# Performance work log

Measured on AMD Instinct MI355X. Metric: run time of the kernel, lower is better.

The kernel has to match this reference:

```python
import jax, jax.numpy as jnp
import numpy as np

N1, N2, P, D = 32, 64, 196, 128


def setup_inputs() -> dict:
    key = jax.random.key(0)
    k1, k2, k3 = jax.random.split(key, 3)
    return {
        "features": jax.random.normal(k1, (N1, P, D), jnp.float32),
        "normal_features": jax.random.normal(k2, (N2, P, D), jnp.float32),
        "background_masks": jax.random.uniform(k3, (N1, P), jnp.float32),
        "PH": 14, "PW": 14, "H": 224, "W": 224,
    }


def _interp1d(x, out_size, axis):
    """1-D bilinear resize along `axis`, matching torch align_corners=False."""
    in_size = x.shape[axis]
    src = jnp.maximum((jnp.arange(out_size) + 0.5) * (in_size / out_size) - 0.5, 0.0)
    i0 = jnp.clip(jnp.floor(src).astype(jnp.int32), 0, in_size - 1)
    i1 = jnp.minimum(i0 + 1, in_size - 1)
    w = (src - i0).astype(x.dtype)
    x0 = jnp.take(x, i0, axis=axis)
    x1 = jnp.take(x, i1, axis=axis)
    shape = [1] * x.ndim
    shape[axis] = out_size
    w = w.reshape(shape)
    return x0 * (1.0 - w) + x1 * w


def reference(features, normal_features, background_masks, PH, PW, H, W):
    # L2-normalize patch features
    f = features / jnp.linalg.norm(features, axis=-1, keepdims=True)      # [N1,P,D]
    nf = normal_features / jnp.linalg.norm(normal_features, axis=-1, keepdims=True)  # [N2,P,D]
    # cdist on unit vectors: ||a-b|| = sqrt(2 - 2 a.b); then /2 as in source
    sim = jnp.einsum('apd,bqd->abpq', f, nf)                              # [N1,N2,P,P]
    dist = jnp.sqrt(jnp.maximum(2.0 - 2.0 * sim, 0.0)) * 0.5
    scores_patch = dist.min(axis=-1)                                      # [N1,N2,P]
    scores_patch = scores_patch * background_masks[:, None, :]
    scores = scores_patch.max(axis=-1)                                    # [N1,N2]
    scores_patch = scores_patch.mean(axis=1)                              # [N1,P]
    n1 = features.shape[0]
    sp = scores_patch.reshape(n1, PH, PW)
    sp = _interp1d(sp, H, axis=1)
    scores_pixel = _interp1d(sp, W, axis=2)                               # [N1,H,W]
    return scores.mean(axis=-1), scores_pixel
```

## Files before the change

kernel.cpp:

```cpp
#include <hip/hip_runtime.h>
#include <hip/hip_fp16.h>

typedef __attribute__((ext_vector_type(8))) short f16x8;
typedef __attribute__((ext_vector_type(8))) _Float16 half8;
typedef __attribute__((ext_vector_type(4))) float f32x4;

__device__ __forceinline__ unsigned short f2h(float x) {
    __half h = __float2half(x);
    unsigned short u;
    __builtin_memcpy(&u, &h, 2);
    return u;
}

__device__ __forceinline__ void gll16(const void* g, void* l) {
    __builtin_amdgcn_global_load_lds(
        (const __attribute__((address_space(1))) unsigned*)g,
        (__attribute__((address_space(3))) unsigned*)l, 16, 0, 0);
}

__global__ __launch_bounds__(256) void norm_kernel(
    const float* __restrict__ feats, const float* __restrict__ nfeats,
    unsigned short* __restrict__ fH, unsigned short* __restrict__ nfH)
{
    int row  = blockIdx.x * 4 + (threadIdx.x >> 6);
    int lane = threadIdx.x & 63;
    const float* src;
    unsigned short* dst;
    if (row < 6272) { src = feats  + (size_t)row * 128; dst = fH  + (size_t)row * 128; }
    else { int r2 = row - 6272; src = nfeats + (size_t)r2 * 128; dst = nfH + (size_t)r2 * 128; }

    float2 v = *(const float2*)(src + lane * 2);
    float ss = v.x * v.x + v.y * v.y;
    #pragma unroll
    for (int m = 1; m < 64; m <<= 1) ss += __shfl_xor(ss, m, 64);
    float rn = rsqrtf(ss);
    ushort2 o; o.x = f2h(v.x * rn); o.y = f2h(v.y * rn);
    *(ushort2*)(dst + lane * 2) = o;
}

__device__ __forceinline__ void stage196(const f16x8* __restrict__ g, f16x8* l,
                                         int tid, int wave) {
    #pragma unroll
    for (int i = 0; i < 6; ++i) {
        int slot = i * 512 + tid;
        int row = slot >> 4, cc = slot & 15;
        gll16(g + row * 16 + (cc ^ (row & 7)), l + i * 512 + wave * 64);
    }
    if (tid < 64) {
        int slot = 3072 + tid;
        int row = slot >> 4, cc = slot & 15;
        gll16(g + row * 16 + (cc ^ (row & 7)), l + 3072);
    }
}

__global__ __launch_bounds__(512, 2) void simmax_kernel(
    const unsigned short* __restrict__ fH, const unsigned short* __restrict__ nfH,
    const float* __restrict__ mask, float* __restrict__ sp, float* __restrict__ scores)
{
    __shared__ f16x8 lds[3 * 3136];
    __shared__ unsigned smaxL[8 * 208];
    __shared__ unsigned scoresL[8];
    f16x8* Fl = lds;
    f16x8* B0 = lds + 3136;
    f16x8* B1 = lds + 6272;

    int a = blockIdx.x & 31, bg = blockIdx.x >> 5;
    int b0 = bg * 8;
    int tid = threadIdx.x, wave = tid >> 6, lane = tid & 63;
    int l15 = lane & 15, lg = lane >> 4;
    int pg = wave & 1, qs = wave >> 1;
    int p0 = pg ? 68 : 0;
    const int qstart[4] = {0, 4, 7, 10};
    const int qend[4]   = {4, 7, 10, 13};

    stage196((const f16x8*)(fH  + (size_t)a  * 196 * 128), Fl, tid, wave);
    stage196((const f16x8*)(nfH + (size_t)b0 * 196 * 128), B0, tid, wave);
    for (int i = tid; i < 8 * 208; i += 512) smaxL[i] = 0u;
    if (tid < 8) scoresL[tid] = 0u;
    __syncthreads();

    half8 pb[8][4];
    #pragma unroll
    for (int pt = 0; pt < 8; ++pt) {
        int row = p0 + pt * 16 + l15;
        #pragma unroll
        for (int ks = 0; ks < 4; ++ks) {
            pb[pt][ks] = *(const half8*)(Fl + ((row << 4) | ((ks * 4 + lg) ^ (row & 7))));
            asm volatile("" : "+v"(pb[pt][ks]));
        }
    }

    for (int bi = 0; bi < 8; ++bi) {
        f16x8* Bcur = (bi & 1) ? B1 : B0;
        f16x8* Bnxt = (bi & 1) ? B0 : B1;
        if (bi < 7)
            stage196((const f16x8*)(nfH + (size_t)(b0 + bi + 1) * 196 * 128), Bnxt, tid, wave);

        float rmax[8];
        #pragma unroll
        for (int pt = 0; pt < 8; ++pt) rmax[pt] = -3.0f;

        for (int qi = qstart[qs]; qi < qend[qs]; ++qi) {
            int qbase = (qi < 12) ? qi * 16 : 180;
            f32x4 acc[8];
            #pragma unroll
            for (int pt = 0; pt < 8; ++pt) acc[pt] = (f32x4){0.f, 0.f, 0.f, 0.f};
            #pragma unroll
            for (int ks = 0; ks < 4; ++ks) {
                int row = qbase + l15;
                half8 qa = *(const half8*)(Bcur + ((row << 4) | ((ks * 4 + lg) ^ (row & 7))));
                #pragma unroll
                for (int pt = 0; pt < 8; ++pt)
                    acc[pt] = __builtin_amdgcn_mfma_f32_16x16x32_f16(qa, pb[pt][ks], acc[pt], 0, 0, 0);
            }
            #pragma unroll
            for (int pt = 0; pt < 8; ++pt)
                rmax[pt] = fmaxf(rmax[pt],
                           fmaxf(fmaxf(acc[pt][0], acc[pt][1]),
                                 fmaxf(acc[pt][2], acc[pt][3])));
        }
        #pragma unroll
        for (int pt = 0; pt < 8; ++pt)
            atomicMax(&smaxL[bi * 208 + p0 + pt * 16 + l15],
                      __float_as_uint(rmax[pt] + 3.0f));

        __syncthreads();
    }

    if (wave < 4) {
        int p = tid;
        float mk = (p < 196) ? mask[a * 196 + p] : 0.0f;
        float d8[8];
        #pragma unroll
        for (int bi = 0; bi < 8; ++bi) {
            float d = 0.0f;
            if (p < 196) {
                float sim = __uint_as_float(smaxL[bi * 208 + p]) - 3.0f;
                d = 0.5f * sqrtf(fmaxf(2.0f - 2.0f * sim, 0.0f)) * mk;
            }
            d8[bi] = d;
            float m = d;
            #pragma unroll
            for (int s = 1; s < 64; s <<= 1) m = fmaxf(m, __shfl_xor(m, s, 64));
            if (lane == 0) atomicMax(&scoresL[bi], __float_as_uint(m));
        }
        if (p < 196) {
            float* dst = sp + ((size_t)a * 196 + p) * 64 + b0;
            *(f32x4*)(dst)     = (f32x4){d8[0], d8[1], d8[2], d8[3]};
            *(f32x4*)(dst + 4) = (f32x4){d8[4], d8[5], d8[6], d8[7]};
        }
    }
    __syncthreads();
    if (tid < 8)
        scores[a * 64 + b0 + tid] = __uint_as_float(scoresL[tid]);
}

__global__ __launch_bounds__(256) void patchmean_kernel(
    const float* __restrict__ sp, const float* __restrict__ scores,
    float* __restrict__ patch, float* __restrict__ out)
{
    int a = blockIdx.x, tid = threadIdx.x;
    if (tid < 196) {
        const f32x4* v = (const f32x4*)(sp + ((size_t)a * 196 + tid) * 64);
        float s = 0.0f;
        #pragma unroll
        for (int j = 0; j < 16; ++j) { f32x4 x = v[j]; s += x[0] + x[1] + x[2] + x[3]; }
        patch[a * 196 + tid] = s * (1.0f / 64.0f);
    }
    if (tid >= 192 && tid < 256) {
        int l = tid - 192;
        float s = scores[a * 64 + l];
        #pragma unroll
        for (int m = 1; m < 64; m <<= 1) s += __shfl_xor(s, m, 64);
        if (l == 0) out[a] = s * (1.0f / 64.0f);
    }
}

__global__ __launch_bounds__(256) void upsample_kernel(
    const float* __restrict__ patch, float* __restrict__ out)
{
    int bid = blockIdx.x;
    int a = bid / 28, band = bid % 28;
    __shared__ float pt[196];
    if (threadIdx.x < 196) pt[threadIdx.x] = patch[a * 196 + threadIdx.x];
    __syncthreads();

    float* op = out + 32 + (size_t)a * 50176 + band * 8 * 224;
    for (int t = threadIdx.x; t < 8 * 224; t += 256) {
        int h = band * 8 + (t / 224), w = t % 224;
        float sh = fmaxf((h + 0.5f) * 0.0625f - 0.5f, 0.0f);
        float sw = fmaxf((w + 0.5f) * 0.0625f - 0.5f, 0.0f);
        int h0 = (int)sh, w0 = (int)sw;
        int h1 = min(h0 + 1, 13), w1 = min(w0 + 1, 13);
        float fh = sh - (float)h0, fw = sw - (float)w0;
        float v00 = pt[h0 * 14 + w0], v01 = pt[h0 * 14 + w1];
        float v10 = pt[h1 * 14 + w0], v11 = pt[h1 * 14 + w1];
        op[t] = (1.0f - fh) * ((1.0f - fw) * v00 + fw * v01)
              +         fh  * ((1.0f - fw) * v10 + fw * v11);
    }
}

extern "C" void kernel_launch(void* const* d_in, const int* in_sizes, int n_in,
                              void* d_out, int out_size, void* d_ws, size_t ws_size,
                              hipStream_t stream) {
    const float* feats  = (const float*)d_in[0];
    const float* nfeats = (const float*)d_in[1];
    const float* mask   = (const float*)d_in[2];
    float* out = (float*)d_out;

    char* w = (char*)d_ws;
    unsigned short* fH  = (unsigned short*)(w);
    unsigned short* nfH = (unsigned short*)(w + 1605632);
    float* sp     = (float*)(w + 4816896);
    float* scores = (float*)(w + 6422528);
    float* patch  = (float*)(w + 6430720);

    norm_kernel<<<4704, 256, 0, stream>>>(feats, nfeats, fH, nfH);
    simmax_kernel<<<256, 512, 0, stream>>>(fH, nfH, mask, sp, scores);
    patchmean_kernel<<<32, 256, 0, stream>>>(sp, scores, patch, out);
    upsample_kernel<<<896, 256, 0, stream>>>(patch, out);
}
```

Baseline: 49.04 us.

## Drop LDS staging in simmax; load MFMA operands directly from global memory

The similarity-max kernel no longer stages features through LDS with async global-to-LDS copies and double buffering. Each lane now reads its MFMA fragments directly from global memory, relying on the L2/L1 caches for the heavy reuse of the normal-feature rows. The work split is also changed: 512 blocks each handle 4 normal images, waves are arranged as 4 patch groups by 2 query halves, and the launch bound now targets higher occupancy. In exchange, global and cache traffic rises and the B operand loads are uncoalesced per-lane 16-byte reads, which may expose memory latency.

Result: slower. 75.87 us (+54.7%).

```diff
diff --git a/kernel.cpp b/kernel.cpp
--- a/kernel.cpp
+++ b/kernel.cpp
@@ -1,7 +1,6 @@
 #include <hip/hip_runtime.h>
 #include <hip/hip_fp16.h>
 
-typedef __attribute__((ext_vector_type(8))) short f16x8;
 typedef __attribute__((ext_vector_type(8))) _Float16 half8;
 typedef __attribute__((ext_vector_type(4))) float f32x4;
 
@@ -10,12 +9,6 @@
     unsigned short u;
     __builtin_memcpy(&u, &h, 2);
     return u;
-}
-
-__device__ __forceinline__ void gll16(const void* g, void* l) {
-    __builtin_amdgcn_global_load_lds(
-        (const __attribute__((address_space(1))) unsigned*)g,
-        (__attribute__((address_space(3))) unsigned*)l, 16, 0, 0);
 }
 
 __global__ __launch_bounds__(256) void norm_kernel(
@@ -38,120 +31,89 @@
     *(ushort2*)(dst + lane * 2) = o;
 }
 
-__device__ __forceinline__ void stage196(const f16x8* __restrict__ g, f16x8* l,
-                                         int tid, int wave) {
-    #pragma unroll
-    for (int i = 0; i < 6; ++i) {
-        int slot = i * 512 + tid;
-        int row = slot >> 4, cc = slot & 15;
-        gll16(g + row * 16 + (cc ^ (row & 7)), l + i * 512 + wave * 64);
-    }
-    if (tid < 64) {
-        int slot = 3072 + tid;
-        int row = slot >> 4, cc = slot & 15;
-        gll16(g + row * 16 + (cc ^ (row & 7)), l + 3072);
-    }
-}
-
-__global__ __launch_bounds__(512, 2) void simmax_kernel(
+__global__ __launch_bounds__(512, 4) void simmax_kernel(
     const unsigned short* __restrict__ fH, const unsigned short* __restrict__ nfH,
     const float* __restrict__ mask, float* __restrict__ sp, float* __restrict__ scores)
 {
-    __shared__ f16x8 lds[3 * 3136];
-    __shared__ unsigned smaxL[8 * 208];
-    __shared__ unsigned scoresL[8];
-    f16x8* Fl = lds;
-    f16x8* B0 = lds + 3136;
-    f16x8* B1 = lds + 6272;
+    __shared__ unsigned smaxL[4 * 208];
+    __shared__ unsigned scoresL[4];
 
-    int a = blockIdx.x & 31, bg = blockIdx.x >> 5;
-    int b0 = bg * 8;
+    int a = blockIdx.x >> 4, bq = blockIdx.x & 15;
+    int b0 = bq * 4;
     int tid = threadIdx.x, wave = tid >> 6, lane = tid & 63;
-    int l15 = lane & 15, lg = lane >> 4;
-    int pg = wave & 1, qs = wave >> 1;
-    int p0 = pg ? 68 : 0;
-    const int qstart[4] = {0, 4, 7, 10};
-    const int qend[4]   = {4, 7, 10, 13};
+    int l15 = lane & 15, lg = (lane >> 4) & 3;
+    int pg = wave & 3, qh = wave >> 2;
+    int p0 = (pg < 3) ? pg * 64 : 132;
 
-    stage196((const f16x8*)(fH  + (size_t)a  * 196 * 128), Fl, tid, wave);
-    stage196((const f16x8*)(nfH + (size_t)b0 * 196 * 128), B0, tid, wave);
-    for (int i = tid; i < 8 * 208; i += 512) smaxL[i] = 0u;
-    if (tid < 8) scoresL[tid] = 0u;
+    for (int i = tid; i < 4 * 208; i += 512) smaxL[i] = 0u;
+    if (tid < 4) scoresL[tid] = 0u;
     __syncthreads();
 
-    half8 pb[8][4];
+    const unsigned short* fbase = fH + (size_t)a * 196 * 128 + l15 * 128 + lg * 8;
+    half8 pb[4][4];
     #pragma unroll
-    for (int pt = 0; pt < 8; ++pt) {
-        int row = p0 + pt * 16 + l15;
+    for (int pt = 0; pt < 4; ++pt) {
         #pragma unroll
         for (int ks = 0; ks < 4; ++ks) {
-            pb[pt][ks] = *(const half8*)(Fl + ((row << 4) | ((ks * 4 + lg) ^ (row & 7))));
+            pb[pt][ks] = *(const half8*)(fbase + (p0 + pt * 16) * 128 + ks * 32);
             asm volatile("" : "+v"(pb[pt][ks]));
         }
     }
 
-    for (int bi = 0; bi < 8; ++bi) {
-        f16x8* Bcur = (bi & 1) ? B1 : B0;
-        f16x8* Bnxt = (bi & 1) ? B0 : B1;
-        if (bi < 7)
-            stage196((const f16x8*)(nfH + (size_t)(b0 + bi + 1) * 196 * 128), Bnxt, tid, wave);
+    int qi0 = qh ? 7 : 0, qi1 = qh ? 13 : 7;
+    for (int bi = 0; bi < 4; ++bi) {
+        const unsigned short* nb = nfH + (size_t)(b0 + bi) * 196 * 128 + l15 * 128 + lg * 8;
+        float rmax[4];
+        #pragma unroll
+        for (int pt = 0; pt < 4; ++pt) rmax[pt] = -3.0f;
 
-        float rmax[8];
-        #pragma unroll
-        for (int pt = 0; pt < 8; ++pt) rmax[pt] = -3.0f;
-
-        for (int qi = qstart[qs]; qi < qend[qs]; ++qi) {
+        for (int qi = qi0; qi < qi1; ++qi) {
             int qbase = (qi < 12) ? qi * 16 : 180;
-            f32x4 acc[8];
+            f32x4 acc[4];
             #pragma unroll
-            for (int pt = 0; pt < 8; ++pt) acc[pt] = (f32x4){0.f, 0.f, 0.f, 0.f};
+            for (int pt = 0; pt < 4; ++pt) acc[pt] = (f32x4){0.f, 0.f, 0.f, 0.f};
             #pragma unroll
             for (int ks = 0; ks < 4; ++ks) {
-                int row = qbase + l15;
-                half8 qa = *(const half8*)(Bcur + ((row << 4) | ((ks * 4 + lg) ^ (row & 7))));
+                half8 qa = *(const half8*)(nb + qbase * 128 + ks * 32);
                 #pragma unroll
-                for (int pt = 0; pt < 8; ++pt)
+                for (int pt = 0; pt < 4; ++pt)
                     acc[pt] = __builtin_amdgcn_mfma_f32_16x16x32_f16(qa, pb[pt][ks], acc[pt], 0, 0, 0);
             }
             #pragma unroll
-            for (int pt = 0; pt < 8; ++pt)
+            for (int pt = 0; pt < 4; ++pt)
                 rmax[pt] = fmaxf(rmax[pt],
                            fmaxf(fmaxf(acc[pt][0], acc[pt][1]),
                                  fmaxf(acc[pt][2], acc[pt][3])));
         }
         #pragma unroll
-        for (int pt = 0; pt < 8; ++pt)
+        for (int pt = 0; pt < 4; ++pt)
             atomicMax(&smaxL[bi * 208 + p0 + pt * 16 + l15],
                       __float_as_uint(rmax[pt] + 3.0f));
+    }
+    __syncthreads();
 
-        __syncthreads();
-    }
-
-    if (wave < 4) {
+    if (tid < 256) {
         int p = tid;
         float mk = (p < 196) ? mask[a * 196 + p] : 0.0f;
-        float d8[8];
+        float d4[4];
         #pragma unroll
-        for (int bi = 0; bi < 8; ++bi) {
+        for (int bi = 0; bi < 4; ++bi) {
             float d = 0.0f;
             if (p < 196) {
                 float sim = __uint_as_float(smaxL[bi * 208 + p]) - 3.0f;
                 d = 0.5f * sqrtf(fmaxf(2.0f - 2.0f * sim, 0.0f)) * mk;
             }
-            d8[bi] = d;
+            d4[bi] = d;
             float m = d;
             #pragma unroll
             for (int s = 1; s < 64; s <<= 1) m = fmaxf(m, __shfl_xor(m, s, 64));
             if (lane == 0) atomicMax(&scoresL[bi], __float_as_uint(m));
         }
-        if (p < 196) {
-            float* dst = sp + ((size_t)a * 196 + p) * 64 + b0;
-            *(f32x4*)(dst)     = (f32x4){d8[0], d8[1], d8[2], d8[3]};
-            *(f32x4*)(dst + 4) = (f32x4){d8[4], d8[5], d8[6], d8[7]};
-        }
+        if (p < 196)
+            *(f32x4*)(sp + ((size_t)a * 196 + p) * 64 + b0) = (f32x4){d4[0], d4[1], d4[2], d4[3]};
     }
     __syncthreads();
-    if (tid < 8)
+    if (tid < 4)
         scores[a * 64 + b0 + tid] = __uint_as_float(scoresL[tid]);
 }
 
@@ -216,7 +178,7 @@
     float* patch  = (float*)(w + 6430720);
 
     norm_kernel<<<4704, 256, 0, stream>>>(feats, nfeats, fH, nfH);
-    simmax_kernel<<<256, 512, 0, stream>>>(fH, nfH, mask, sp, scores);
+    simmax_kernel<<<512, 512, 0, stream>>>(fH, nfH, mask, sp, scores);
     patchmean_kernel<<<32, 256, 0, stream>>>(sp, scores, patch, out);
     upsample_kernel<<<896, 256, 0, stream>>>(patch, out);
 }
```
